# Kernel tuning notes

Measured on AMD Instinct MI355X. Metric: run time of the kernel, lower is better.

Reference implementation:

```python
import jax, jax.numpy as jnp
import numpy as np

B, T, D, H = 2, 2048, 1024, 16
DH = D // H
EPS = 1e-3  # keras LayerNormalization default epsilon


def setup_inputs() -> dict:
    key = jax.random.key(0)
    ks = jax.random.split(key, 10)
    s = 1.0 / np.sqrt(D)
    return {
        "x": jax.random.normal(ks[0], (B, T, D), jnp.float32),
        "wq": jax.random.normal(ks[1], (D, D), jnp.float32) * s,
        "bq": jnp.zeros((D,), jnp.float32),
        "wk": jax.random.normal(ks[2], (D, D), jnp.float32) * s,
        "bk": jnp.zeros((D,), jnp.float32),
        "wv": jax.random.normal(ks[3], (D, D), jnp.float32) * s,
        "bv": jnp.zeros((D,), jnp.float32),
        "wo": jax.random.normal(ks[4], (D, D), jnp.float32) * s,
        "bo": jnp.zeros((D,), jnp.float32),
        "scale": jnp.asarray(1.0, jnp.float32),  # learnable scalar, init 1.0
        "gamma": jnp.ones((D,), jnp.float32),
        "beta": jnp.zeros((D,), jnp.float32),
    }


def _split_heads(t):
    # [B,T,D] -> [B,T,H,DH] -> [H,B,T,DH]; head h takes channels h*DH:(h+1)*DH,
    # matching tf.concat(tf.split(t, H, axis=-1), axis=0) up to batch layout.
    return t.reshape(B, T, H, DH).transpose(2, 0, 1, 3)


def reference(x, wq, bq, wk, bk, wv, bv, wo, bo, scale, gamma, beta):
    q = _split_heads(x @ wq + bq)  # [H,B,T,DH]
    k = _split_heads(x @ wk + bk)
    v = _split_heads(x @ wv + bv)
    scores = scale * jnp.einsum("hbqd,hbkd->hbqk", q, k)  # [H,B,Tq,Tk]
    attn = jax.nn.softmax(scores, axis=-1)
    ctx = jnp.einsum("hbqk,hbkd->hbqd", attn, v)  # [H,B,T,DH]
    # inverse of split: heads back to last dim in head order
    merged = ctx.transpose(1, 2, 0, 3).reshape(B, T, D)
    out = merged @ wo + bo
    out = out + x  # residual connection
    mean = jnp.mean(out, axis=-1, keepdims=True)
    var = jnp.var(out, axis=-1, keepdims=True)
    out = (out - mean) * jax.lax.rsqrt(var + EPS) * gamma + beta
    return out
```

## Files before the change

### kernel.cpp

```cpp
#include <hip/hip_runtime.h>
#include <hip/hip_bf16.h>

#define B_ 2
#define T_ 2048
#define D_ 1024
#define H_ 16
#define M_ (B_ * T_)

typedef __attribute__((ext_vector_type(4))) float f32x4;
typedef __attribute__((ext_vector_type(8))) short s16x8;
typedef __attribute__((ext_vector_type(4))) short s16x4;

__device__ __forceinline__ short f2bs(float f) {
  unsigned u = __builtin_bit_cast(unsigned, f);
  u += 0x7fffu + ((u >> 16) & 1u);
  return (short)(u >> 16);
}
__device__ __forceinline__ unsigned pack2bf(float lo, float hi) {
  unsigned a = (unsigned short)f2bs(lo);
  unsigned b = (unsigned short)f2bs(hi);
  return a | (b << 16);
}

__global__ __launch_bounds__(256) void cvt_f32_bf16(const float* __restrict__ in,
                                                    short* __restrict__ out, int n4) {
  int i = blockIdx.x * 256 + threadIdx.x;
  if (i < n4) {
    float4 v = ((const float4*)in)[i];
    s16x4 o;
    o.x = f2bs(v.x); o.y = f2bs(v.y); o.z = f2bs(v.z); o.w = f2bs(v.w);
    ((s16x4*)out)[i] = o;
  }
}

__global__ __launch_bounds__(256) void cvt_transpose(
    const float* __restrict__ w0, const float* __restrict__ w1,
    const float* __restrict__ w2, const float* __restrict__ w3,
    short* __restrict__ o0, short* __restrict__ o1,
    short* __restrict__ o2, short* __restrict__ o3) {
  __shared__ float tile[64][65];
  const float* W; short* Wt;
  if (blockIdx.z == 0) { W = w0; Wt = o0; }
  else if (blockIdx.z == 1) { W = w1; Wt = o1; }
  else if (blockIdx.z == 2) { W = w2; Wt = o2; }
  else { W = w3; Wt = o3; }
  const int k0 = blockIdx.x * 64, n0 = blockIdx.y * 64;
  const int t = threadIdx.x;
  const int c = t & 63, r4 = t >> 6;
#pragma unroll
  for (int i = 0; i < 16; ++i) {
    int row = i * 4 + r4;
    tile[row][c] = W[(size_t)(k0 + row) * D_ + n0 + c];
  }
  __syncthreads();
#pragma unroll
  for (int i = 0; i < 16; ++i) {
    int row = i * 4 + r4;
    Wt[(size_t)(n0 + row) * D_ + k0 + c] = f2bs(tile[c][row]);
  }
}

template <int MODE>
__device__ __forceinline__ void gemm_core(short As[128][72], short Bs[128][72],
                                          const short* __restrict__ A,
                                          const short* __restrict__ Wt,
                                          const float* __restrict__ bias,
                                          const float* __restrict__ resid,
                                          void* __restrict__ outp) {
  const int t = threadIdx.x;
  const int lane = t & 63, wid = t >> 6;
  const int l15 = lane & 15, g = lane >> 4;
  const int wr = wid >> 1, wc = wid & 1;
  const int n0 = blockIdx.x * 128;
  const int m0 = blockIdx.y * 128;

  const f32x4 fz = {0.f, 0.f, 0.f, 0.f};
  f32x4 acc[4][4];
#pragma unroll
  for (int m = 0; m < 4; ++m)
#pragma unroll
    for (int n = 0; n < 4; ++n) acc[m][n] = fz;

  const int srow = t >> 1, shalf = (t & 1) * 32;
  const short* ap = A + (size_t)(m0 + srow) * D_ + shalf;
  const short* bp = Wt + (size_t)(n0 + srow) * D_ + shalf;

  s16x8 ar[4], br[4];
#pragma unroll
  for (int c = 0; c < 4; ++c) {
    ar[c] = *(const s16x8*)(ap + c * 8);
    br[c] = *(const s16x8*)(bp + c * 8);
  }

  for (int k0 = 0; k0 < D_; k0 += 64) {
    __syncthreads();
#pragma unroll
    for (int c = 0; c < 4; ++c) {
      *(s16x8*)&As[srow][shalf + c * 8] = ar[c];
      *(s16x8*)&Bs[srow][shalf + c * 8] = br[c];
    }
    __syncthreads();
    if (k0 + 64 < D_) {
#pragma unroll
      for (int c = 0; c < 4; ++c) {
        ar[c] = *(const s16x8*)(ap + k0 + 64 + c * 8);
        br[c] = *(const s16x8*)(bp + k0 + 64 + c * 8);
      }
    }
#pragma unroll
    for (int kk = 0; kk < 64; kk += 32) {
      s16x8 af[4], bfr[4];
#pragma unroll
      for (int m = 0; m < 4; ++m)
        af[m] = *(const s16x8*)&As[wr * 64 + m * 16 + l15][kk + g * 8];
#pragma unroll
      for (int n = 0; n < 4; ++n)
        bfr[n] = *(const s16x8*)&Bs[wc * 64 + n * 16 + l15][kk + g * 8];
#pragma unroll
      for (int m = 0; m < 4; ++m)
#pragma unroll
        for (int n = 0; n < 4; ++n)
          acc[m][n] = __builtin_amdgcn_mfma_f32_16x16x32_bf16(af[m], bfr[n], acc[m][n], 0, 0, 0);
    }
  }

#pragma unroll
  for (int m = 0; m < 4; ++m) {
#pragma unroll
    for (int n = 0; n < 4; ++n) {
      const int col = n0 + wc * 64 + n * 16 + l15;
      const float bv = bias[col];
#pragma unroll
      for (int i = 0; i < 4; ++i) {
        const int row = m0 + wr * 64 + m * 16 + g * 4 + i;
        float v = acc[m][n][i] + bv;
        if (MODE == 1) {
          ((float*)outp)[(size_t)row * D_ + col] = v + resid[(size_t)row * D_ + col];
        } else {
          ((short*)outp)[(size_t)row * D_ + col] = f2bs(v);
        }
      }
    }
  }
}

__global__ __launch_bounds__(256) void gemm_qkv_kernel(
    const short* __restrict__ xb, const short* __restrict__ wq,
    const short* __restrict__ wk, const short* __restrict__ wv,
    const float* __restrict__ bq, const float* __restrict__ bk,
    const float* __restrict__ bv, short* __restrict__ Qb, short* __restrict__ Kb,
    short* __restrict__ Vb) {
  __shared__ __align__(16) short As[128][72];
  __shared__ __align__(16) short Bs[128][72];
  const short* W;
  const float* bias;
  short* out;
  if (blockIdx.z == 0) { W = wq; bias = bq; out = Qb; }
  else if (blockIdx.z == 1) { W = wk; bias = bk; out = Kb; }
  else { W = wv; bias = bv; out = Vb; }
  gemm_core<0>(As, Bs, xb, W, bias, nullptr, out);
}

__global__ __launch_bounds__(256) void gemm_out_kernel(
    const short* __restrict__ ctx, const short* __restrict__ wo,
    const float* __restrict__ bo, const float* __restrict__ x,
    float* __restrict__ out) {
  __shared__ __align__(16) short As[128][72];
  __shared__ __align__(16) short Bs[128][72];
  gemm_core<1>(As, Bs, ctx, wo, bo, x, out);
}

__global__ __launch_bounds__(256) void attn_kernel(
    const short* __restrict__ Qb, const short* __restrict__ Kb,
    const short* __restrict__ Vb, const float* __restrict__ scale_p,
    short* __restrict__ ctx) {
  __shared__ __align__(16) short Ks[64][72];
  __shared__ __align__(16) unsigned Vt[64][36];
  __shared__ __align__(16) unsigned Ps[4][16][36];

  const int qt = blockIdx.x, h = blockIdx.y, b = blockIdx.z;
  const int hc = h * 64;
  const size_t tokbase = (size_t)b * T_;
  const float scale = *scale_p;
  const int t = threadIdx.x, lane = t & 63, wid = t >> 6;
  const int l15 = lane & 15, g = lane >> 4;
  const int wq0 = wid * 16;

  const short* qp = Qb + (tokbase + (size_t)qt * 64 + wq0 + l15) * D_ + hc + g * 8;
  s16x8 qf0 = *(const s16x8*)qp;
  s16x8 qf1 = *(const s16x8*)(qp + 32);

  const int krow = t >> 2, kcol = (t & 3) * 16;
  const int va = t >> 3, vd0 = (t & 7) * 8;
  const int vswz = (t & 7) << 2;
  const short* kp = Kb + (tokbase + krow) * D_ + hc + kcol;
  const short* vp = Vb + (tokbase + 2 * (size_t)va) * D_ + hc + vd0;

  s16x8 kr0 = *(const s16x8*)kp;
  s16x8 kr1 = *(const s16x8*)(kp + 8);
  s16x8 vr0 = *(const s16x8*)vp;
  s16x8 vr1 = *(const s16x8*)(vp + D_);

  const f32x4 fz = {0.f, 0.f, 0.f, 0.f};
  f32x4 acc[4];
#pragma unroll
  for (int m = 0; m < 4; ++m) acc[m] = fz;
  float mrun = -__builtin_inff(), lrun = 0.f;

  for (int kt = 0; kt < T_ / 64; ++kt) {
    __syncthreads();
    *(s16x8*)&Ks[krow][kcol] = kr0;
    *(s16x8*)&Ks[krow][kcol + 8] = kr1;
#pragma unroll
    for (int j = 0; j < 8; ++j) {
      unsigned pk = (unsigned)(unsigned short)vr0[j] |
                    ((unsigned)(unsigned short)vr1[j] << 16);
      Vt[vd0 + j][va ^ vswz] = pk;
    }
    __syncthreads();
    if (kt + 1 < T_ / 64) {
      const short* kp2 = kp + (size_t)(kt + 1) * 64 * D_;
      kr0 = *(const s16x8*)kp2;
      kr1 = *(const s16x8*)(kp2 + 8);
      const short* vp2 = vp + (size_t)(kt + 1) * 64 * D_;
      vr0 = *(const s16x8*)vp2;
      vr1 = *(const s16x8*)(vp2 + D_);
    }

    f32x4 s[4];
#pragma unroll
    for (int m = 0; m < 4; ++m) s[m] = fz;
#pragma unroll
    for (int m = 0; m < 4; ++m) {
      s16x8 kf = *(const s16x8*)&Ks[m * 16 + l15][g * 8];
      s[m] = __builtin_amdgcn_mfma_f32_16x16x32_bf16(kf, qf0, s[m], 0, 0, 0);
    }
#pragma unroll
    for (int m = 0; m < 4; ++m) {
      s16x8 kf = *(const s16x8*)&Ks[m * 16 + l15][32 + g * 8];
      s[m] = __builtin_amdgcn_mfma_f32_16x16x32_bf16(kf, qf1, s[m], 0, 0, 0);
    }

    float pm = -__builtin_inff();
#pragma unroll
    for (int m = 0; m < 4; ++m)
#pragma unroll
      for (int i = 0; i < 4; ++i) {
        float v = s[m][i] * scale;
        s[m][i] = v;
        pm = fmaxf(pm, v);
      }
    pm = fmaxf(pm, __shfl_xor(pm, 16));
    pm = fmaxf(pm, __shfl_xor(pm, 32));
    float mnew = fmaxf(mrun, pm);
    float corr = __expf(mrun - mnew);
    float rs = 0.f;
#pragma unroll
    for (int m = 0; m < 4; ++m)
#pragma unroll
      for (int i = 0; i < 4; ++i) {
        float p = __expf(s[m][i] - mnew);
        s[m][i] = p;
        rs += p;
      }
    rs += __shfl_xor(rs, 16);
    rs += __shfl_xor(rs, 32);
    lrun = lrun * corr + rs;
    mrun = mnew;
#pragma unroll
    for (int m = 0; m < 4; ++m)
#pragma unroll
      for (int i = 0; i < 4; ++i) acc[m][i] *= corr;

#pragma unroll
    for (int m = 0; m < 4; ++m) {
      Ps[wid][l15][m * 8 + g * 2 + 0] = pack2bf(s[m][0], s[m][1]);
      Ps[wid][l15][m * 8 + g * 2 + 1] = pack2bf(s[m][2], s[m][3]);
    }

#pragma unroll
    for (int k2 = 0; k2 < 2; ++k2) {
      s16x8 bp2 = *(const s16x8*)&Ps[wid][l15][k2 * 16 + g * 4];
#pragma unroll
      for (int m = 0; m < 4; ++m) {
        int swq = (k2 * 4 + g) ^ (m * 2 + (l15 >> 3));
        s16x8 av = *(const s16x8*)&Vt[m * 16 + l15][swq * 4];
        acc[m] = __builtin_amdgcn_mfma_f32_16x16x32_bf16(av, bp2, acc[m], 0, 0, 0);
      }
    }
  }

  float inv = 1.f / lrun;
  short* cp = ctx + (tokbase + (size_t)qt * 64 + wq0 + l15) * D_ + hc;
#pragma unroll
  for (int m = 0; m < 4; ++m) {
    s16x4 o;
    o.x = f2bs(acc[m][0] * inv);
    o.y = f2bs(acc[m][1] * inv);
    o.z = f2bs(acc[m][2] * inv);
    o.w = f2bs(acc[m][3] * inv);
    *(s16x4*)(cp + m * 16 + g * 4) = o;
  }
}

__global__ __launch_bounds__(256) void ln_kernel(float* __restrict__ out,
                                                 const float* __restrict__ gamma,
                                                 const float* __restrict__ beta) {
  __shared__ float reds[4], redss[4];
  const size_t row = blockIdx.x;
  float* p = out + row * D_;
  const int t = threadIdx.x;
  float4 v = ((const float4*)p)[t];
  float s = v.x + v.y + v.z + v.w;
  float ss = v.x * v.x + v.y * v.y + v.z * v.z + v.w * v.w;
#pragma unroll
  for (int off = 1; off < 64; off <<= 1) {
    s += __shfl_xor(s, off);
    ss += __shfl_xor(ss, off);
  }
  const int wid = t >> 6, lane = t & 63;
  if (lane == 0) { reds[wid] = s; redss[wid] = ss; }
  __syncthreads();
  float S = reds[0] + reds[1] + reds[2] + reds[3];
  float SS = redss[0] + redss[1] + redss[2] + redss[3];
  const float mean = S * (1.f / D_);
  const float var = SS * (1.f / D_) - mean * mean;
  const float r = rsqrtf(var + 1e-3f);
  float4 gm = ((const float4*)gamma)[t];
  float4 bt = ((const float4*)beta)[t];
  float4 o;
  o.x = (v.x - mean) * r * gm.x + bt.x;
  o.y = (v.y - mean) * r * gm.y + bt.y;
  o.z = (v.z - mean) * r * gm.z + bt.z;
  o.w = (v.w - mean) * r * gm.w + bt.w;
  ((float4*)p)[t] = o;
}

extern "C" void kernel_launch(void* const* d_in, const int* in_sizes, int n_in,
                              void* d_out, int out_size, void* d_ws, size_t ws_size,
                              hipStream_t stream) {
  const float* x = (const float*)d_in[0];
  const float* wq = (const float*)d_in[1];
  const float* bq = (const float*)d_in[2];
  const float* wk = (const float*)d_in[3];
  const float* bk = (const float*)d_in[4];
  const float* wv = (const float*)d_in[5];
  const float* bv = (const float*)d_in[6];
  const float* wo = (const float*)d_in[7];
  const float* bo = (const float*)d_in[8];
  const float* scale = (const float*)d_in[9];
  const float* gamma = (const float*)d_in[10];
  const float* beta = (const float*)d_in[11];
  float* out = (float*)d_out;

  short* xb = (short*)d_ws;
  short* wqt = xb + (size_t)M_ * D_;
  short* wkt = wqt + (size_t)D_ * D_;
  short* wvt = wkt + (size_t)D_ * D_;
  short* wot = wvt + (size_t)D_ * D_;
  short* Qb = wot + (size_t)D_ * D_;
  short* Kb = Qb + (size_t)M_ * D_;
  short* Vb = Kb + (size_t)M_ * D_;
  short* ctx = Vb + (size_t)M_ * D_;

  const int n4x = M_ * D_ / 4;
  cvt_f32_bf16<<<dim3((n4x + 255) / 256), 256, 0, stream>>>(x, xb, n4x);
  cvt_transpose<<<dim3(16, 16, 4), 256, 0, stream>>>(wq, wk, wv, wo, wqt, wkt, wvt, wot);

  gemm_qkv_kernel<<<dim3(D_ / 128, M_ / 128, 3), 256, 0, stream>>>(
      xb, wqt, wkt, wvt, bq, bk, bv, Qb, Kb, Vb);

  attn_kernel<<<dim3(T_ / 64, H_, B_), 256, 0, stream>>>(Qb, Kb, Vb, scale, ctx);

  gemm_out_kernel<<<dim3(D_ / 128, M_ / 128), 256, 0, stream>>>(ctx, wot, bo, x, out);

  ln_kernel<<<dim3(M_), 256, 0, stream>>>(out, gamma, beta);
}
```

Baseline: 157.2 us.

## Fold softmax scale and log2e into Q projection, use exp2 with lazy rescale

The softmax scale and log2(e) are folded into the Q projection epilogue, so the attention loop drops its per-score multiply and uses native exp2. The running-max rescale of the accumulator is skipped unless some lane's max grows by more than 8 (in log2 units), which cuts the corr multiplies. P packing uses the hardware v_cvt_pk_bf16_f32 instruction, and the V transpose uses byte-permute instead of per-element shifts. Rounding Q after scaling slightly changes numerics, and lazy rescaling lets exponent values reach up to 2^8 before renormalising, which is safe only within fp32/bf16 range.

```diff
diff --git a/kernel.cpp b/kernel.cpp
--- a/kernel.cpp
+++ b/kernel.cpp
@@ -10,16 +10,17 @@
 typedef __attribute__((ext_vector_type(4))) float f32x4;
 typedef __attribute__((ext_vector_type(8))) short s16x8;
 typedef __attribute__((ext_vector_type(4))) short s16x4;
+typedef __attribute__((ext_vector_type(4))) unsigned u32x4;
 
 __device__ __forceinline__ short f2bs(float f) {
   unsigned u = __builtin_bit_cast(unsigned, f);
   u += 0x7fffu + ((u >> 16) & 1u);
   return (short)(u >> 16);
 }
-__device__ __forceinline__ unsigned pack2bf(float lo, float hi) {
-  unsigned a = (unsigned short)f2bs(lo);
-  unsigned b = (unsigned short)f2bs(hi);
-  return a | (b << 16);
+__device__ __forceinline__ unsigned cvt_pk_bf16(float lo, float hi) {
+  unsigned r;
+  asm("v_cvt_pk_bf16_f32 %0, %1, %2" : "=v"(r) : "v"(lo), "v"(hi));
+  return r;
 }
 
 __global__ __launch_bounds__(256) void cvt_f32_bf16(const float* __restrict__ in,
@@ -66,7 +67,7 @@
                                           const short* __restrict__ Wt,
                                           const float* __restrict__ bias,
                                           const float* __restrict__ resid,
-                                          void* __restrict__ outp) {
+                                          void* __restrict__ outp, float mult) {
   const int t = threadIdx.x;
   const int lane = t & 63, wid = t >> 6;
   const int l15 = lane & 15, g = lane >> 4;
@@ -137,7 +138,7 @@
         if (MODE == 1) {
           ((float*)outp)[(size_t)row * D_ + col] = v + resid[(size_t)row * D_ + col];
         } else {
-          ((short*)outp)[(size_t)row * D_ + col] = f2bs(v);
+          ((short*)outp)[(size_t)row * D_ + col] = f2bs(v * mult);
         }
       }
     }
@@ -148,17 +149,18 @@
     const short* __restrict__ xb, const short* __restrict__ wq,
     const short* __restrict__ wk, const short* __restrict__ wv,
     const float* __restrict__ bq, const float* __restrict__ bk,
-    const float* __restrict__ bv, short* __restrict__ Qb, short* __restrict__ Kb,
-    short* __restrict__ Vb) {
+    const float* __restrict__ bv, const float* __restrict__ scale_p,
+    short* __restrict__ Qb, short* __restrict__ Kb, short* __restrict__ Vb) {
   __shared__ __align__(16) short As[128][72];
   __shared__ __align__(16) short Bs[128][72];
   const short* W;
   const float* bias;
   short* out;
-  if (blockIdx.z == 0) { W = wq; bias = bq; out = Qb; }
+  float mult = 1.0f;
+  if (blockIdx.z == 0) { W = wq; bias = bq; out = Qb; mult = scale_p[0] * 1.44269504f; }
   else if (blockIdx.z == 1) { W = wk; bias = bk; out = Kb; }
   else { W = wv; bias = bv; out = Vb; }
-  gemm_core<0>(As, Bs, xb, W, bias, nullptr, out);
+  gemm_core<0>(As, Bs, xb, W, bias, nullptr, out, mult);
 }
 
 __global__ __launch_bounds__(256) void gemm_out_kernel(
@@ -167,13 +169,12 @@
     float* __restrict__ out) {
   __shared__ __align__(16) short As[128][72];
   __shared__ __align__(16) short Bs[128][72];
-  gemm_core<1>(As, Bs, ctx, wo, bo, x, out);
+  gemm_core<1>(As, Bs, ctx, wo, bo, x, out, 1.0f);
 }
 
 __global__ __launch_bounds__(256) void attn_kernel(
     const short* __restrict__ Qb, const short* __restrict__ Kb,
-    const short* __restrict__ Vb, const float* __restrict__ scale_p,
-    short* __restrict__ ctx) {
+    const short* __restrict__ Vb, short* __restrict__ ctx) {
   __shared__ __align__(16) short Ks[64][72];
   __shared__ __align__(16) unsigned Vt[64][36];
   __shared__ __align__(16) unsigned Ps[4][16][36];
@@ -181,7 +182,6 @@
   const int qt = blockIdx.x, h = blockIdx.y, b = blockIdx.z;
   const int hc = h * 64;
   const size_t tokbase = (size_t)b * T_;
-  const float scale = *scale_p;
   const int t = threadIdx.x, lane = t & 63, wid = t >> 6;
   const int l15 = lane & 15, g = lane >> 4;
   const int wq0 = wid * 16;
@@ -205,17 +205,21 @@
   f32x4 acc[4];
 #pragma unroll
   for (int m = 0; m < 4; ++m) acc[m] = fz;
-  float mrun = -__builtin_inff(), lrun = 0.f;
+  float mrun = -3.0e38f, lrun = 0.f;
 
   for (int kt = 0; kt < T_ / 64; ++kt) {
     __syncthreads();
     *(s16x8*)&Ks[krow][kcol] = kr0;
     *(s16x8*)&Ks[krow][kcol + 8] = kr1;
-#pragma unroll
-    for (int j = 0; j < 8; ++j) {
-      unsigned pk = (unsigned)(unsigned short)vr0[j] |
-                    ((unsigned)(unsigned short)vr1[j] << 16);
-      Vt[vd0 + j][va ^ vswz] = pk;
+    {
+      u32x4 v0d = __builtin_bit_cast(u32x4, vr0);
+      u32x4 v1d = __builtin_bit_cast(u32x4, vr1);
+#pragma unroll
+      for (int jd = 0; jd < 4; ++jd) {
+        unsigned lo = v0d[jd], hi = v1d[jd];
+        Vt[vd0 + 2 * jd][va ^ vswz] = __builtin_amdgcn_perm(hi, lo, 0x05040100u);
+        Vt[vd0 + 2 * jd + 1][va ^ vswz] = __builtin_amdgcn_perm(hi, lo, 0x07060302u);
+      }
     }
     __syncthreads();
     if (kt + 1 < T_ / 64) {
@@ -241,42 +245,40 @@
       s[m] = __builtin_amdgcn_mfma_f32_16x16x32_bf16(kf, qf1, s[m], 0, 0, 0);
     }
 
-    float pm = -__builtin_inff();
-#pragma unroll
-    for (int m = 0; m < 4; ++m)
-#pragma unroll
-      for (int i = 0; i < 4; ++i) {
-        float v = s[m][i] * scale;
-        s[m][i] = v;
-        pm = fmaxf(pm, v);
-      }
+    float pm = -3.0e38f;
+#pragma unroll
+    for (int m = 0; m < 4; ++m) {
+      float a = fmaxf(s[m][0], s[m][1]);
+      float c = fmaxf(s[m][2], s[m][3]);
+      pm = fmaxf(pm, fmaxf(a, c));
+    }
     pm = fmaxf(pm, __shfl_xor(pm, 16));
     pm = fmaxf(pm, __shfl_xor(pm, 32));
-    float mnew = fmaxf(mrun, pm);
-    float corr = __expf(mrun - mnew);
-    float rs = 0.f;
-#pragma unroll
-    for (int m = 0; m < 4; ++m)
-#pragma unroll
-      for (int i = 0; i < 4; ++i) {
-        float p = __expf(s[m][i] - mnew);
-        s[m][i] = p;
-        rs += p;
-      }
+    if (__any(pm > mrun + 8.f)) {
+      float mnew = fmaxf(mrun, pm);
+      float corr = __builtin_amdgcn_exp2f(mrun - mnew);
+#pragma unroll
+      for (int m = 0; m < 4; ++m)
+#pragma unroll
+        for (int i = 0; i < 4; ++i) acc[m][i] *= corr;
+      lrun *= corr;
+      mrun = mnew;
+    }
+    float rs0 = 0.f, rs1 = 0.f;
+#pragma unroll
+    for (int m = 0; m < 4; ++m) {
+      float p0 = __builtin_amdgcn_exp2f(s[m][0] - mrun);
+      float p1 = __builtin_amdgcn_exp2f(s[m][1] - mrun);
+      float p2 = __builtin_amdgcn_exp2f(s[m][2] - mrun);
+      float p3 = __builtin_amdgcn_exp2f(s[m][3] - mrun);
+      rs0 += p0 + p2; rs1 += p1 + p3;
+      Ps[wid][l15][m * 8 + g * 2 + 0] = cvt_pk_bf16(p0, p1);
+      Ps[wid][l15][m * 8 + g * 2 + 1] = cvt_pk_bf16(p2, p3);
+    }
+    float rs = rs0 + rs1;
     rs += __shfl_xor(rs, 16);
     rs += __shfl_xor(rs, 32);
-    lrun = lrun * corr + rs;
-    mrun = mnew;
-#pragma unroll
-    for (int m = 0; m < 4; ++m)
-#pragma unroll
-      for (int i = 0; i < 4; ++i) acc[m][i] *= corr;
-
-#pragma unroll
-    for (int m = 0; m < 4; ++m) {
-      Ps[wid][l15][m * 8 + g * 2 + 0] = pack2bf(s[m][0], s[m][1]);
-      Ps[wid][l15][m * 8 + g * 2 + 1] = pack2bf(s[m][2], s[m][3]);
-    }
+    lrun += rs;
 
 #pragma unroll
     for (int k2 = 0; k2 < 2; ++k2) {
@@ -368,9 +370,9 @@
   cvt_transpose<<<dim3(16, 16, 4), 256, 0, stream>>>(wq, wk, wv, wo, wqt, wkt, wvt, wot);
 
   gemm_qkv_kernel<<<dim3(D_ / 128, M_ / 128, 3), 256, 0, stream>>>(
-      xb, wqt, wkt, wvt, bq, bk, bv, Qb, Kb, Vb);
-
-  attn_kernel<<<dim3(T_ / 64, H_, B_), 256, 0, stream>>>(Qb, Kb, Vb, scale, ctx);
+      xb, wqt, wkt, wvt, bq, bk, bv, scale, Qb, Kb, Vb);
+
+  attn_kernel<<<dim3(T_ / 64, H_, B_), 256, 0, stream>>>(Qb, Kb, Vb, ctx);
 
   gemm_out_kernel<<<dim3(D_ / 128, M_ / 128), 256, 0, stream>>>(ctx, wot, bo, x, out);
 
```

After: 149.9 us. 1.05x faster.
